# Kernel tuning notes

Hardware: AMD Instinct MI355X
Metric: run time of the kernel (lower is better)

## Reference

```python
import jax, jax.numpy as jnp
import numpy as np

B, C, Q, T, D = 16, 6, 256, 256, 256
NUM_IDS = 300
IMG_H = IMG_W = 512


def setup_inputs() -> dict:
    key = jax.random.key(0)
    ks = jax.random.split(key, 8)
    det_tokens = jax.random.normal(ks[0], (B, C, Q, D), jnp.float32)
    det_scores = jax.random.uniform(ks[1], (B, C, Q), jnp.float32)
    det_boxes = jax.random.uniform(ks[2], (B, C, Q, 4), jnp.float32)
    assoc = jax.nn.softmax(jax.random.normal(ks[3], (B, C, Q, T), jnp.float32), axis=-1)
    cam_mask = jax.random.uniform(ks[4], (B, C)) < 0.9
    target_mask = jax.random.uniform(ks[5], (B, C, Q)) < 0.5
    ids = jax.random.randint(ks[6], (B, C, Q), 0, NUM_IDS)
    boxes = jax.random.uniform(ks[7], (B, C, Q, 4), jnp.float32) * IMG_W
    return {"det_tokens": det_tokens, "det_scores": det_scores, "det_boxes": det_boxes,
            "assoc": assoc, "boxes": boxes, "cam_mask": cam_mask,
            "target_mask": target_mask, "ids": ids, "img_h": IMG_H, "img_w": IMG_W}


def _masked_mean(x, m):
    w = m.astype(x.dtype)
    return (x * w).sum() / jnp.maximum(w.sum(), 1.0)


def _pack(ids, target_mask, cam_mask, q_count):
    # Vectorized version of _query_ids_from_targets: stable-compact valid targets
    # to the front of the query axis (preserves original order, as boolean indexing does).
    order = jnp.argsort(jnp.where(target_mask, 0, 1), axis=-1, stable=True)  # valid first
    sids = jnp.take_along_axis(ids, order, axis=-1)[..., :q_count]
    count = target_mask.sum(axis=-1)  # [B,C]
    qvalid = (jnp.arange(q_count)[None, None, :] < count[..., None]) & cam_mask[..., None]
    qids = jnp.where(qvalid, sids, -1)
    return qids, qvalid, order


def reference(det_tokens, det_scores, det_boxes, assoc, boxes, cam_mask, target_mask, ids, img_h, img_w):
    Bq, Cc, Qn, Tn = assoc.shape
    qids, qvalid, order = _pack(ids, target_mask, cam_mask, Qn)

    # det_norm
    det_norm = jnp.mean(det_tokens ** 2)

    # detector supervision (masked BCE on scores + masked L1 on boxes)
    norm = jnp.array([img_w, img_h, img_w, img_h], det_boxes.dtype)
    box_gt = boxes / norm  # [B,C,maxT,4]
    sboxes = jnp.take_along_axis(box_gt, order[..., None], axis=2)[:, :, :Qn]
    obj_target = qvalid.astype(det_scores.dtype)
    box_target = jnp.where(qvalid[..., None], jnp.clip(sboxes, 0.0, 1.0), 0.0)
    p = jnp.clip(det_scores, 1e-6, 1.0 - 1e-6)
    bce = -(obj_target * jnp.log(p) + (1.0 - obj_target) * jnp.log1p(-p))
    cam3 = jnp.broadcast_to(cam_mask[:, :, None], bce.shape)
    score_loss = _masked_mean(bce, cam3)
    box_loss = _masked_mean(jnp.abs(det_boxes - box_target),
                            jnp.broadcast_to(qvalid[..., None], det_boxes.shape))
    det_supervision = score_loss + box_loss

    # assoc entropy (masked by camera validity)
    logp_full = jnp.log(jnp.maximum(assoc, 1e-8))
    entropy = -(logp_full * assoc).sum(-1)  # [B,C,Q]
    assoc_entropy_loss = _masked_mean(entropy, jnp.broadcast_to(cam_mask[:, :, None], entropy.shape))

    # assoc supervised NLL over track slots
    slots = jnp.remainder(jnp.maximum(qids, 0), Tn)  # [B,C,Q]
    nll = -jnp.take_along_axis(logp_full, slots[..., None], axis=-1)[..., 0]
    assoc_pair_loss = _masked_mean(nll, qvalid)

    # cross-view consistency: broadcasted id-equality replaces quadruple python loop
    eq = qids[:, :, None, :, None] == qids[:, None, :, None, :]       # [B,c1,c2,q1,q2]
    pv = qvalid[:, :, None, :, None] & qvalid[:, None, :, None, :]
    tri = jnp.triu(jnp.ones((Cc, Cc), bool), 1)[None, :, :, None, None]  # c1 < c2
    M = (eq & pv & tri).astype(assoc.dtype)
    cnt = M.sum(-1)  # [B,c1,c2,q1]
    peer = jnp.einsum('bcdqp,bdpt->bcdqt', M, assoc) / jnp.maximum(cnt, 1.0)[..., None]
    ref = assoc[:, :, None, :, :]
    term = jnp.mean((ref - peer) ** 2, axis=-1)  # per-pair MSE over track slots
    assoc_consistency = _masked_mean(term, cnt > 0)

    total = det_norm + det_supervision + assoc_entropy_loss + assoc_pair_loss + assoc_consistency
    return total, det_norm, det_supervision, assoc_entropy_loss, assoc_pair_loss, assoc_consistency
```

## Files before the change

### kernel.cpp

```cpp
#include <hip/hip_runtime.h>
#include <math.h>

#define BB 16
#define CC 6
#define QQ 256
#define TT 256
#define DD 256
#define NPAIR 15
#define NBC (BB * CC)
#define CONS_BLOCKS (BB * NPAIR * 4)
#define PACK_BLOCKS NBC
#define BIG_BLOCKS (NBC * 8)
#define MAIN_BLOCKS (CONS_BLOCKS + PACK_BLOCKS + BIG_BLOCKS)


__device__ __forceinline__ float block_sum256(float v, float* s_red) {
    #pragma unroll
    for (int off = 32; off > 0; off >>= 1) v += __shfl_xor(v, off, 64);
    __syncthreads();
    if ((threadIdx.x & 63) == 0) s_red[threadIdx.x >> 6] = v;
    __syncthreads();
    return s_red[0] + s_red[1] + s_red[2] + s_red[3];
}

__device__ __forceinline__ float2 block_sum256x2(float a, float b, float2* s_red2) {
    #pragma unroll
    for (int off = 32; off > 0; off >>= 1) {
        a += __shfl_xor(a, off, 64);
        b += __shfl_xor(b, off, 64);
    }
    __syncthreads();
    if ((threadIdx.x & 63) == 0) s_red2[threadIdx.x >> 6] = make_float2(a, b);
    __syncthreads();
    float2 r;
    r.x = s_red2[0].x + s_red2[1].x + s_red2[2].x + s_red2[3].x;
    r.y = s_red2[0].y + s_red2[1].y + s_red2[2].y + s_red2[3].y;
    return r;
}

__device__ __forceinline__ int read_bool(const void* p, int idx, int fmt) {
    if (fmt == 2) return ((const float*)p)[idx] != 0.0f;
    if (fmt == 1) return ((const unsigned char*)p)[idx] != 0;
    return ((const int*)p)[idx] != 0;
}

__device__ __forceinline__ int detect_fmt(const void* tm_raw, int* s_cf, int* s_cm) {
    const int t = threadIdx.x;
    if (t == 0) { *s_cf = 0; *s_cm = 0; }
    __syncthreads();
    uint4 w = ((const uint4*)tm_raw)[t];
    unsigned int u4[4] = {w.x, w.y, w.z, w.w};
    int cf = 0, cm = 0;
    #pragma unroll
    for (int k = 0; k < 4; k++) {
        cf += ((u4[k] >> 24) == 0x3Fu);
        cm += ((u4[k] & 0xFFFFFF00u) != 0u);
    }
    if (cf) atomicAdd(s_cf, cf);
    if (cm) atomicAdd(s_cm, cm);
    __syncthreads();
    return (*s_cf > 16) ? 2 : ((*s_cm > 0) ? 1 : 0);
}

__device__ __forceinline__ int block_pack(const void* tm_raw,
                                          const int* __restrict__ ids,
                                          int bc, int fmt, int cam,
                                          int* s_sids, int* s_wsum,
                                          int* s_out) {
    const int t = threadIdx.x, lane = t & 63, wv = t >> 6;
    const int tm = read_bool(tm_raw, bc * QQ + t, fmt);
    int v = tm;
    #pragma unroll
    for (int off = 1; off < 64; off <<= 1) {
        int u = __shfl_up(v, off, 64);
        if (lane >= off) v += u;
    }
    if (lane == 63) s_wsum[wv] = v;
    __syncthreads();
    const int count = s_wsum[0] + s_wsum[1] + s_wsum[2] + s_wsum[3];
    int woff = 0;
    #pragma unroll
    for (int k = 0; k < 3; k++) woff += (k < wv) ? s_wsum[k] : 0;
    const int excl = woff + v - tm;
    const int rank = tm ? excl : (count + (t - excl));
    s_sids[rank] = ids[bc * QQ + t];
    __syncthreads();
    s_out[t] = (t < count && cam) ? s_sids[t] : -1;
    __syncthreads();
    return count;
}

__global__ __launch_bounds__(256)
void k_main(const float4* __restrict__ tok,
            const float* __restrict__ assoc,
            const float* __restrict__ det_scores,
            const float* __restrict__ det_boxes,
            const float* __restrict__ boxes,
            const void* __restrict__ cam_raw,
            const void* __restrict__ tm_raw,
            const int* __restrict__ ids,
            const int* __restrict__ img_h_p,
            const int* __restrict__ img_w_p,
            float* __restrict__ packPart,
            float* __restrict__ bigPart,
            float* __restrict__ consPart) {
    const int blk = blockIdx.x;
    const int t = threadIdx.x, lane = t & 63, wv = t >> 6;
    __shared__ int s_cf, s_cm;
    __shared__ float2 s_red2[4];

    if (blk >= CONS_BLOCKS + PACK_BLOCKS) {
        const int bb = blk - (CONS_BLOCKS + PACK_BLOCKS);
        const int bc = bb >> 3;
        const long base = (long)bc * 16384 + (long)(bb & 7) * 2048 + t;
        const float4* asc = (const float4*)assoc;
        const int fmt = detect_fmt(tm_raw, &s_cf, &s_cm);
        const int cam = read_bool(cam_raw, bc, fmt);

        float ss = 0.0f, ent = 0.0f;
        #pragma unroll
        for (int h = 0; h < 2; h++) {
            const long o = base + h * 1024;
            float4 t0 = tok[o], t1 = tok[o + 256], t2 = tok[o + 512], t3 = tok[o + 768];
            float4 a0 = asc[o], a1 = asc[o + 256], a2 = asc[o + 512], a3 = asc[o + 768];
            ss += t0.x * t0.x + t0.y * t0.y + t0.z * t0.z + t0.w * t0.w
                + t1.x * t1.x + t1.y * t1.y + t1.z * t1.z + t1.w * t1.w
                + t2.x * t2.x + t2.y * t2.y + t2.z * t2.z + t2.w * t2.w
                + t3.x * t3.x + t3.y * t3.y + t3.z * t3.z + t3.w * t3.w;
            if (cam) {
                ent -= a0.x * __logf(fmaxf(a0.x, 1e-8f)) + a0.y * __logf(fmaxf(a0.y, 1e-8f))
                     + a0.z * __logf(fmaxf(a0.z, 1e-8f)) + a0.w * __logf(fmaxf(a0.w, 1e-8f));
                ent -= a1.x * __logf(fmaxf(a1.x, 1e-8f)) + a1.y * __logf(fmaxf(a1.y, 1e-8f))
                     + a1.z * __logf(fmaxf(a1.z, 1e-8f)) + a1.w * __logf(fmaxf(a1.w, 1e-8f));
                ent -= a2.x * __logf(fmaxf(a2.x, 1e-8f)) + a2.y * __logf(fmaxf(a2.y, 1e-8f))
                     + a2.z * __logf(fmaxf(a2.z, 1e-8f)) + a2.w * __logf(fmaxf(a2.w, 1e-8f));
                ent -= a3.x * __logf(fmaxf(a3.x, 1e-8f)) + a3.y * __logf(fmaxf(a3.y, 1e-8f))
                     + a3.z * __logf(fmaxf(a3.z, 1e-8f)) + a3.w * __logf(fmaxf(a3.w, 1e-8f));
            }
        }
        float2 r = block_sum256x2(ss, ent, s_red2);
        if (t == 0) { bigPart[bb * 2] = r.x; bigPart[bb * 2 + 1] = r.y; }

    } else if (blk >= CONS_BLOCKS) {
        const int bc = blk - CONS_BLOCKS;
        __shared__ int s_sids[QQ], s_qid[QQ], s_wsum[4];
        const int fmt = detect_fmt(tm_raw, &s_cf, &s_cm);
        const int cam = read_bool(cam_raw, bc, fmt);
        const int count = block_pack(tm_raw, ids, bc, fmt, cam, s_sids, s_wsum, s_qid);
        const int tm = read_bool(tm_raw, bc * QQ + t, fmt);
        int v = tm;
        #pragma unroll
        for (int off = 1; off < 64; off <<= 1) {
            int u = __shfl_up(v, off, 64);
            if (lane >= off) v += u;
        }
        int woff = 0;
        #pragma unroll
        for (int k = 0; k < 3; k++) woff += (k < wv) ? s_wsum[k] : 0;
        const int excl = woff + v - tm;
        const int rank = tm ? excl : (count + (t - excl));

        const int j = t;
        const int qv = (j < count) && cam;
        const int qid = s_qid[j];

        float score_sum = 0.0f, box_sum = 0.0f, pair_sum = 0.0f;
        if (cam) {
            float p = det_scores[(size_t)bc * QQ + j];
            p = fminf(fmaxf(p, 1e-6f), 1.0f - 1e-6f);
            score_sum = (j < count) ? -__logf(p) : -__logf(1.0f - p);
        }
        if (qv) {
            int slot = qid & (TT - 1);
            float a = assoc[((size_t)bc * QQ + j) * TT + slot];
            pair_sum = -__logf(fmaxf(a, 1e-8f));
        }
        if (tm && cam) {
            const int jj = rank;
            const float iw = (float)img_w_p[0], ih = (float)img_h_p[0];
            const float* bx = boxes + ((size_t)bc * QQ + t) * 4;
            const float* db = det_boxes + ((size_t)bc * QQ + jj) * 4;
            float b0 = fminf(fmaxf(bx[0] / iw, 0.0f), 1.0f);
            float b1 = fminf(fmaxf(bx[1] / ih, 0.0f), 1.0f);
            float b2 = fminf(fmaxf(bx[2] / iw, 0.0f), 1.0f);
            float b3 = fminf(fmaxf(bx[3] / ih, 0.0f), 1.0f);
            box_sum = fabsf(db[0] - b0) + fabsf(db[1] - b1) +
                      fabsf(db[2] - b2) + fabsf(db[3] - b3);
        }
        float2 r1 = block_sum256x2(score_sum, box_sum, s_red2);
        float2 r2 = block_sum256x2(pair_sum, 0.0f, s_red2);
        if (t == 0) {
            float* row = packPart + bc * 8;
            row[0] = r1.x; row[1] = r1.y; row[2] = r2.x;
            row[3] = cam ? (float)count : 0.0f;
            row[4] = (float)cam;
        }

    } else {
        const int cb = blk;
        const int qg = cb & 3;
        const int bp = cb >> 2;
        const int b = bp / NPAIR;
        int pi = bp % NPAIR;
        int c = 0, d = 1;
        {
            int k = pi;
            for (c = 0; c < CC - 1; c++) {
                int span = CC - 1 - c;
                if (k < span) { d = c + 1 + k; break; }
                k -= span;
            }
        }
        __shared__ int s_sids[QQ], s_qc[QQ], s_qd[QQ], s_wsum[4];
        const int fmt = detect_fmt(tm_raw, &s_cf, &s_cm);
        const int cam_c = read_bool(cam_raw, b * CC + c, fmt);
        const int cam_d = read_bool(cam_raw, b * CC + d, fmt);
        block_pack(tm_raw, ids, b * CC + c, fmt, cam_c, s_sids, s_wsum, s_qc);
        block_pack(tm_raw, ids, b * CC + d, fmt, cam_d, s_sids, s_wsum, s_qd);

        const int qd0 = s_qd[lane];
        const int qd1 = s_qd[64 + lane];
        const int qd2 = s_qd[128 + lane];
        const int qd3 = s_qd[192 + lane];
        int idarr[16];
        #pragma unroll
        for (int qi = 0; qi < 16; qi++) idarr[qi] = s_qc[qg * 64 + wv * 16 + qi];

        const float4* assoc_c = (const float4*)(assoc + (size_t)(b * CC + c) * QQ * TT);
        const float4* assoc_d = (const float4*)(assoc + (size_t)(b * CC + d) * QQ * TT);

        float tot = 0.0f, nval = 0.0f;
        #pragma unroll 4
        for (int qi = 0; qi < 16; qi++) {
            const int id = idarr[qi];
            if (id < 0) continue;
            unsigned long long m0 = __ballot(qd0 == id);
            unsigned long long m1 = __ballot(qd1 == id);
            unsigned long long m2 = __ballot(qd2 == id);
            unsigned long long m3 = __ballot(qd3 == id);
            int cnt = __popcll(m0) + __popcll(m1) + __popcll(m2) + __popcll(m3);
            if (cnt == 0) continue;
            const int q = qg * 64 + wv * 16 + qi;
            float4 r = assoc_c[(size_t)q * (TT / 4) + lane];
            float ax = 0.0f, ay = 0.0f, az = 0.0f, aw = 0.0f;
            unsigned long long mm[4] = {m0, m1, m2, m3};
            #pragma unroll
            for (int kk = 0; kk < 4; kk++) {
                unsigned long long m = mm[kk];
                while (m) {
                    int p = kk * 64 + __builtin_ctzll(m);
                    m &= m - 1;
                    float4 vv = assoc_d[(size_t)p * (TT / 4) + lane];
                    ax += vv.x; ay += vv.y; az += vv.z; aw += vv.w;
                }
            }
            float inv = 1.0f / (float)cnt;
            float dx = r.x - ax * inv, dy = r.y - ay * inv;
            float dz = r.z - az * inv, dw = r.w - aw * inv;
            tot += dx * dx + dy * dy + dz * dz + dw * dw;
            nval += 1.0f;
        }
        float2 r2 = block_sum256x2(tot, nval, s_red2);
        if (t == 0) {
            consPart[cb * 2] = r2.x * (1.0f / TT);
            consPart[cb * 2 + 1] = r2.y;
        }
    }
}

__global__ __launch_bounds__(256)
void k_fin(const float* __restrict__ packPart, const float2* __restrict__ bigPart,
           const float2* __restrict__ consPart, float* __restrict__ out) {
    const int t = threadIdx.x;
    __shared__ float s_red[4];
    float sc = 0, bx = 0, pr = 0, qv = 0, cm = 0;
    if (t < NBC) {
        const float* row = packPart + t * 8;
        sc = row[0]; bx = row[1]; pr = row[2]; qv = row[3]; cm = row[4];
    }
    float ss = 0, ent = 0;
    #pragma unroll
    for (int k = 0; k < BIG_BLOCKS / 256; k++) {
        float2 v = bigPart[k * 256 + t];
        ss += v.x; ent += v.y;
    }
    float cons = 0, nval = 0;
    for (int i = t; i < CONS_BLOCKS; i += 256) {
        float2 v = consPart[i];
        cons += v.x; nval += v.y;
    }
    sc = block_sum256(sc, s_red);
    bx = block_sum256(bx, s_red);
    pr = block_sum256(pr, s_red);
    qv = block_sum256(qv, s_red);
    cm = block_sum256(cm, s_red);
    ss = block_sum256(ss, s_red);
    ent = block_sum256(ent, s_red);
    cons = block_sum256(cons, s_red);
    nval = block_sum256(nval, s_red);
    if (t == 0) {
        float det_norm = ss / (float)((long)BB * CC * QQ * DD);
        float denom_cam = fmaxf(cm * (float)QQ, 1.0f);
        float score_loss = sc / denom_cam;
        float box_loss = bx / fmaxf(4.0f * qv, 1.0f);
        float det_sup = score_loss + box_loss;
        float ent_loss = ent / denom_cam;
        float pair_loss = pr / fmaxf(qv, 1.0f);
        float cons_loss = cons / fmaxf(nval, 1.0f);
        out[0] = det_norm + det_sup + ent_loss + pair_loss + cons_loss;
        out[1] = det_norm;
        out[2] = det_sup;
        out[3] = ent_loss;
        out[4] = pair_loss;
        out[5] = cons_loss;
    }
}

extern "C" void kernel_launch(void* const* d_in, const int* in_sizes, int n_in,
                              void* d_out, int out_size, void* d_ws, size_t ws_size,
                              hipStream_t stream) {
    const float* det_tokens = (const float*)d_in[0];
    const float* det_scores = (const float*)d_in[1];
    const float* det_boxes  = (const float*)d_in[2];
    const float* assoc      = (const float*)d_in[3];
    const float* boxes      = (const float*)d_in[4];
    const void*  cam_raw    = d_in[5];
    const void*  tm_raw     = d_in[6];
    const int*   ids        = (const int*)d_in[7];
    const int*   img_h      = (const int*)d_in[8];
    const int*   img_w      = (const int*)d_in[9];

    char* ws = (char*)d_ws;
    float* packPart = (float*)(ws + 0);
    float* bigPart  = (float*)(ws + 4096);
    float* consPart = (float*)(ws + 16384);

    k_main<<<MAIN_BLOCKS, 256, 0, stream>>>((const float4*)det_tokens, assoc,
                                            det_scores, det_boxes, boxes,
                                            cam_raw, tm_raw, ids, img_h, img_w,
                                            packPart, bigPart, consPart);
    k_fin<<<1, 256, 0, stream>>>(packPart, (const float2*)bigPart,
                                 (const float2*)consPart, (float*)d_out);
}
```

Baseline: 112.4 us.

## Reorder block roles, wave-level format detection, fused pack scans and reductions

Block roles are reordered so the bandwidth-heavy streaming blocks come first, followed by consistency blocks and then pack blocks. The shared-memory atomic format detection is replaced with per-wave ballots, which removes two barriers from every block. The two prefix-sum packs in consistency blocks are fused into one pass, det_tokens is read with nontemporal loads, assoc loads are skipped for inactive cameras, and the final and pack reductions are merged into single multi-value reductions. These cut barrier and latency overhead, at the cost of more code and register pressure.

```diff
diff --git a/kernel.cpp b/kernel.cpp
--- a/kernel.cpp
+++ b/kernel.cpp
@@ -8,11 +8,13 @@
 #define DD 256
 #define NPAIR 15
 #define NBC (BB * CC)
-#define CONS_BLOCKS (BB * NPAIR * 4)
-#define PACK_BLOCKS NBC
-#define BIG_BLOCKS (NBC * 8)
-#define MAIN_BLOCKS (CONS_BLOCKS + PACK_BLOCKS + BIG_BLOCKS)
-
+#define BIGB (NBC * 8)
+#define CONSB (BB * NPAIR * 4)
+#define PACKB NBC
+#define MAIN_BLOCKS (BIGB + CONSB + PACKB)
+
+
+typedef float f4 __attribute__((ext_vector_type(4)));
 
 __device__ __forceinline__ float block_sum256(float v, float* s_red) {
     #pragma unroll
@@ -38,60 +40,88 @@
     return r;
 }
 
+__device__ __forceinline__ float4 block_sum256x4(float a, float b, float c,
+                                                 float d, float4* s_red4) {
+    #pragma unroll
+    for (int off = 32; off > 0; off >>= 1) {
+        a += __shfl_xor(a, off, 64);
+        b += __shfl_xor(b, off, 64);
+        c += __shfl_xor(c, off, 64);
+        d += __shfl_xor(d, off, 64);
+    }
+    __syncthreads();
+    if ((threadIdx.x & 63) == 0) s_red4[threadIdx.x >> 6] = make_float4(a, b, c, d);
+    __syncthreads();
+    float4 r;
+    r.x = s_red4[0].x + s_red4[1].x + s_red4[2].x + s_red4[3].x;
+    r.y = s_red4[0].y + s_red4[1].y + s_red4[2].y + s_red4[3].y;
+    r.z = s_red4[0].z + s_red4[1].z + s_red4[2].z + s_red4[3].z;
+    r.w = s_red4[0].w + s_red4[1].w + s_red4[2].w + s_red4[3].w;
+    return r;
+}
+
 __device__ __forceinline__ int read_bool(const void* p, int idx, int fmt) {
     if (fmt == 2) return ((const float*)p)[idx] != 0.0f;
     if (fmt == 1) return ((const unsigned char*)p)[idx] != 0;
     return ((const int*)p)[idx] != 0;
 }
 
-__device__ __forceinline__ int detect_fmt(const void* tm_raw, int* s_cf, int* s_cm) {
-    const int t = threadIdx.x;
-    if (t == 0) { *s_cf = 0; *s_cm = 0; }
-    __syncthreads();
-    uint4 w = ((const uint4*)tm_raw)[t];
-    unsigned int u4[4] = {w.x, w.y, w.z, w.w};
-    int cf = 0, cm = 0;
-    #pragma unroll
-    for (int k = 0; k < 4; k++) {
-        cf += ((u4[k] >> 24) == 0x3Fu);
-        cm += ((u4[k] & 0xFFFFFF00u) != 0u);
-    }
-    if (cf) atomicAdd(s_cf, cf);
-    if (cm) atomicAdd(s_cm, cm);
-    __syncthreads();
-    return (*s_cf > 16) ? 2 : ((*s_cm > 0) ? 1 : 0);
-}
-
-__device__ __forceinline__ int block_pack(const void* tm_raw,
-                                          const int* __restrict__ ids,
-                                          int bc, int fmt, int cam,
-                                          int* s_sids, int* s_wsum,
-                                          int* s_out) {
+__device__ __forceinline__ int detect_fmt_wave(const void* tm_raw) {
+    const int lane = threadIdx.x & 63;
+    uint4 w = ((const uint4*)tm_raw)[lane];
+    unsigned long long f0 = __ballot((w.x >> 24) == 0x3Fu);
+    unsigned long long f1 = __ballot((w.y >> 24) == 0x3Fu);
+    unsigned long long f2 = __ballot((w.z >> 24) == 0x3Fu);
+    unsigned long long f3 = __ballot((w.w >> 24) == 0x3Fu);
+    int cf = __popcll(f0) + __popcll(f1) + __popcll(f2) + __popcll(f3);
+    unsigned long long m0 = __ballot((w.x & 0xFFFFFF00u) != 0u);
+    unsigned long long m1 = __ballot((w.y & 0xFFFFFF00u) != 0u);
+    unsigned long long m2 = __ballot((w.z & 0xFFFFFF00u) != 0u);
+    unsigned long long m3 = __ballot((w.w & 0xFFFFFF00u) != 0u);
+    int cm = __popcll(m0) | __popcll(m1) | __popcll(m2) | __popcll(m3);
+    return (cf > 16) ? 2 : ((cm > 0) ? 1 : 0);
+}
+
+__device__ __forceinline__ void block_pack2(const void* tm_raw,
+                                            const int* __restrict__ ids,
+                                            int bc_c, int bc_d, int fmt,
+                                            int cam_c, int cam_d,
+                                            int* s_tmp, int* s_wsum,
+                                            int* s_qc, int* s_qd,
+                                            int& count_c, int& count_d) {
     const int t = threadIdx.x, lane = t & 63, wv = t >> 6;
-    const int tm = read_bool(tm_raw, bc * QQ + t, fmt);
-    int v = tm;
+    const int tmc = read_bool(tm_raw, bc_c * QQ + t, fmt);
+    const int tmd = read_bool(tm_raw, bc_d * QQ + t, fmt);
+    int vc = tmc, vd = tmd;
     #pragma unroll
     for (int off = 1; off < 64; off <<= 1) {
-        int u = __shfl_up(v, off, 64);
-        if (lane >= off) v += u;
-    }
-    if (lane == 63) s_wsum[wv] = v;
-    __syncthreads();
-    const int count = s_wsum[0] + s_wsum[1] + s_wsum[2] + s_wsum[3];
-    int woff = 0;
-    #pragma unroll
-    for (int k = 0; k < 3; k++) woff += (k < wv) ? s_wsum[k] : 0;
-    const int excl = woff + v - tm;
-    const int rank = tm ? excl : (count + (t - excl));
-    s_sids[rank] = ids[bc * QQ + t];
-    __syncthreads();
-    s_out[t] = (t < count && cam) ? s_sids[t] : -1;
-    __syncthreads();
-    return count;
+        int uc = __shfl_up(vc, off, 64);
+        int ud = __shfl_up(vd, off, 64);
+        if (lane >= off) { vc += uc; vd += ud; }
+    }
+    if (lane == 63) { s_wsum[wv] = vc; s_wsum[4 + wv] = vd; }
+    __syncthreads();
+    count_c = s_wsum[0] + s_wsum[1] + s_wsum[2] + s_wsum[3];
+    count_d = s_wsum[4] + s_wsum[5] + s_wsum[6] + s_wsum[7];
+    int woc = 0, wod = 0;
+    #pragma unroll
+    for (int k = 0; k < 3; k++) {
+        if (k < wv) { woc += s_wsum[k]; wod += s_wsum[4 + k]; }
+    }
+    const int exc = woc + vc - tmc;
+    const int exd = wod + vd - tmd;
+    const int rc = tmc ? exc : (count_c + (t - exc));
+    const int rd = tmd ? exd : (count_d + (t - exd));
+    s_tmp[rc] = ids[bc_c * QQ + t];
+    s_tmp[QQ + rd] = ids[bc_d * QQ + t];
+    __syncthreads();
+    s_qc[t] = (t < count_c && cam_c) ? s_tmp[t] : -1;
+    s_qd[t] = (t < count_d && cam_d) ? s_tmp[QQ + t] : -1;
+    __syncthreads();
 }
 
 __global__ __launch_bounds__(256)
-void k_main(const float4* __restrict__ tok,
+void k_main(const f4* __restrict__ tok,
             const float* __restrict__ assoc,
             const float* __restrict__ det_scores,
             const float* __restrict__ det_boxes,
@@ -106,28 +136,30 @@
             float* __restrict__ consPart) {
     const int blk = blockIdx.x;
     const int t = threadIdx.x, lane = t & 63, wv = t >> 6;
-    __shared__ int s_cf, s_cm;
     __shared__ float2 s_red2[4];
 
-    if (blk >= CONS_BLOCKS + PACK_BLOCKS) {
-        const int bb = blk - (CONS_BLOCKS + PACK_BLOCKS);
+    if (blk < BIGB) {
+        const int bb = blk;
         const int bc = bb >> 3;
         const long base = (long)bc * 16384 + (long)(bb & 7) * 2048 + t;
-        const float4* asc = (const float4*)assoc;
-        const int fmt = detect_fmt(tm_raw, &s_cf, &s_cm);
+        const f4* asc = (const f4*)assoc;
+        const int fmt = detect_fmt_wave(tm_raw);
         const int cam = read_bool(cam_raw, bc, fmt);
 
         float ss = 0.0f, ent = 0.0f;
         #pragma unroll
         for (int h = 0; h < 2; h++) {
             const long o = base + h * 1024;
-            float4 t0 = tok[o], t1 = tok[o + 256], t2 = tok[o + 512], t3 = tok[o + 768];
-            float4 a0 = asc[o], a1 = asc[o + 256], a2 = asc[o + 512], a3 = asc[o + 768];
+            f4 t0 = __builtin_nontemporal_load(&tok[o]);
+            f4 t1 = __builtin_nontemporal_load(&tok[o + 256]);
+            f4 t2 = __builtin_nontemporal_load(&tok[o + 512]);
+            f4 t3 = __builtin_nontemporal_load(&tok[o + 768]);
             ss += t0.x * t0.x + t0.y * t0.y + t0.z * t0.z + t0.w * t0.w
                 + t1.x * t1.x + t1.y * t1.y + t1.z * t1.z + t1.w * t1.w
                 + t2.x * t2.x + t2.y * t2.y + t2.z * t2.z + t2.w * t2.w
                 + t3.x * t3.x + t3.y * t3.y + t3.z * t3.z + t3.w * t3.w;
             if (cam) {
+                f4 a0 = asc[o], a1 = asc[o + 256], a2 = asc[o + 512], a3 = asc[o + 768];
                 ent -= a0.x * __logf(fmaxf(a0.x, 1e-8f)) + a0.y * __logf(fmaxf(a0.y, 1e-8f))
                      + a0.z * __logf(fmaxf(a0.z, 1e-8f)) + a0.w * __logf(fmaxf(a0.w, 1e-8f));
                 ent -= a1.x * __logf(fmaxf(a1.x, 1e-8f)) + a1.y * __logf(fmaxf(a1.y, 1e-8f))
@@ -141,63 +173,8 @@
         float2 r = block_sum256x2(ss, ent, s_red2);
         if (t == 0) { bigPart[bb * 2] = r.x; bigPart[bb * 2 + 1] = r.y; }
 
-    } else if (blk >= CONS_BLOCKS) {
-        const int bc = blk - CONS_BLOCKS;
-        __shared__ int s_sids[QQ], s_qid[QQ], s_wsum[4];
-        const int fmt = detect_fmt(tm_raw, &s_cf, &s_cm);
-        const int cam = read_bool(cam_raw, bc, fmt);
-        const int count = block_pack(tm_raw, ids, bc, fmt, cam, s_sids, s_wsum, s_qid);
-        const int tm = read_bool(tm_raw, bc * QQ + t, fmt);
-        int v = tm;
-        #pragma unroll
-        for (int off = 1; off < 64; off <<= 1) {
-            int u = __shfl_up(v, off, 64);
-            if (lane >= off) v += u;
-        }
-        int woff = 0;
-        #pragma unroll
-        for (int k = 0; k < 3; k++) woff += (k < wv) ? s_wsum[k] : 0;
-        const int excl = woff + v - tm;
-        const int rank = tm ? excl : (count + (t - excl));
-
-        const int j = t;
-        const int qv = (j < count) && cam;
-        const int qid = s_qid[j];
-
-        float score_sum = 0.0f, box_sum = 0.0f, pair_sum = 0.0f;
-        if (cam) {
-            float p = det_scores[(size_t)bc * QQ + j];
-            p = fminf(fmaxf(p, 1e-6f), 1.0f - 1e-6f);
-            score_sum = (j < count) ? -__logf(p) : -__logf(1.0f - p);
-        }
-        if (qv) {
-            int slot = qid & (TT - 1);
-            float a = assoc[((size_t)bc * QQ + j) * TT + slot];
-            pair_sum = -__logf(fmaxf(a, 1e-8f));
-        }
-        if (tm && cam) {
-            const int jj = rank;
-            const float iw = (float)img_w_p[0], ih = (float)img_h_p[0];
-            const float* bx = boxes + ((size_t)bc * QQ + t) * 4;
-            const float* db = det_boxes + ((size_t)bc * QQ + jj) * 4;
-            float b0 = fminf(fmaxf(bx[0] / iw, 0.0f), 1.0f);
-            float b1 = fminf(fmaxf(bx[1] / ih, 0.0f), 1.0f);
-            float b2 = fminf(fmaxf(bx[2] / iw, 0.0f), 1.0f);
-            float b3 = fminf(fmaxf(bx[3] / ih, 0.0f), 1.0f);
-            box_sum = fabsf(db[0] - b0) + fabsf(db[1] - b1) +
-                      fabsf(db[2] - b2) + fabsf(db[3] - b3);
-        }
-        float2 r1 = block_sum256x2(score_sum, box_sum, s_red2);
-        float2 r2 = block_sum256x2(pair_sum, 0.0f, s_red2);
-        if (t == 0) {
-            float* row = packPart + bc * 8;
-            row[0] = r1.x; row[1] = r1.y; row[2] = r2.x;
-            row[3] = cam ? (float)count : 0.0f;
-            row[4] = (float)cam;
-        }
-
-    } else {
-        const int cb = blk;
+    } else if (blk < BIGB + CONSB) {
+        const int cb = blk - BIGB;
         const int qg = cb & 3;
         const int bp = cb >> 2;
         const int b = bp / NPAIR;
@@ -211,12 +188,13 @@
                 k -= span;
             }
         }
-        __shared__ int s_sids[QQ], s_qc[QQ], s_qd[QQ], s_wsum[4];
-        const int fmt = detect_fmt(tm_raw, &s_cf, &s_cm);
+        __shared__ int s_tmp[2 * QQ], s_qc[QQ], s_qd[QQ], s_wsum[8];
+        const int fmt = detect_fmt_wave(tm_raw);
         const int cam_c = read_bool(cam_raw, b * CC + c, fmt);
         const int cam_d = read_bool(cam_raw, b * CC + d, fmt);
-        block_pack(tm_raw, ids, b * CC + c, fmt, cam_c, s_sids, s_wsum, s_qc);
-        block_pack(tm_raw, ids, b * CC + d, fmt, cam_d, s_sids, s_wsum, s_qd);
+        int count_c, count_d;
+        block_pack2(tm_raw, ids, b * CC + c, b * CC + d, fmt, cam_c, cam_d,
+                    s_tmp, s_wsum, s_qc, s_qd, count_c, count_d);
 
         const int qd0 = s_qd[lane];
         const int qd1 = s_qd[64 + lane];
@@ -226,8 +204,8 @@
         #pragma unroll
         for (int qi = 0; qi < 16; qi++) idarr[qi] = s_qc[qg * 64 + wv * 16 + qi];
 
-        const float4* assoc_c = (const float4*)(assoc + (size_t)(b * CC + c) * QQ * TT);
-        const float4* assoc_d = (const float4*)(assoc + (size_t)(b * CC + d) * QQ * TT);
+        const f4* assoc_c = (const f4*)(assoc + (size_t)(b * CC + c) * QQ * TT);
+        const f4* assoc_d = (const f4*)(assoc + (size_t)(b * CC + d) * QQ * TT);
 
         float tot = 0.0f, nval = 0.0f;
         #pragma unroll 4
@@ -241,7 +219,7 @@
             int cnt = __popcll(m0) + __popcll(m1) + __popcll(m2) + __popcll(m3);
             if (cnt == 0) continue;
             const int q = qg * 64 + wv * 16 + qi;
-            float4 r = assoc_c[(size_t)q * (TT / 4) + lane];
+            f4 r = assoc_c[(size_t)q * (TT / 4) + lane];
             float ax = 0.0f, ay = 0.0f, az = 0.0f, aw = 0.0f;
             unsigned long long mm[4] = {m0, m1, m2, m3};
             #pragma unroll
@@ -250,7 +228,7 @@
                 while (m) {
                     int p = kk * 64 + __builtin_ctzll(m);
                     m &= m - 1;
-                    float4 vv = assoc_d[(size_t)p * (TT / 4) + lane];
+                    f4 vv = assoc_d[(size_t)p * (TT / 4) + lane];
                     ax += vv.x; ay += vv.y; az += vv.z; aw += vv.w;
                 }
             }
@@ -265,40 +243,111 @@
             consPart[cb * 2] = r2.x * (1.0f / TT);
             consPart[cb * 2 + 1] = r2.y;
         }
+
+    } else {
+        const int bc = blk - (BIGB + CONSB);
+        __shared__ int s_sids[QQ], s_wsum[4];
+        __shared__ float4 s_red4[4];
+        const int fmt = detect_fmt_wave(tm_raw);
+        const int cam = read_bool(cam_raw, bc, fmt);
+
+        const int tm = read_bool(tm_raw, bc * QQ + t, fmt);
+        int v = tm;
+        #pragma unroll
+        for (int off = 1; off < 64; off <<= 1) {
+            int u = __shfl_up(v, off, 64);
+            if (lane >= off) v += u;
+        }
+        if (lane == 63) s_wsum[wv] = v;
+        __syncthreads();
+        const int count = s_wsum[0] + s_wsum[1] + s_wsum[2] + s_wsum[3];
+        int woff = 0;
+        #pragma unroll
+        for (int k = 0; k < 3; k++) woff += (k < wv) ? s_wsum[k] : 0;
+        const int excl = woff + v - tm;
+        const int rank = tm ? excl : (count + (t - excl));
+        s_sids[rank] = ids[bc * QQ + t];
+        __syncthreads();
+
+        const int j = t;
+        const int qv = (j < count) && cam;
+        const int qid = qv ? s_sids[j] : -1;
+
+        float score_sum = 0.0f, box_sum = 0.0f, pair_sum = 0.0f;
+        if (cam) {
+            float p = det_scores[(size_t)bc * QQ + j];
+            p = fminf(fmaxf(p, 1e-6f), 1.0f - 1e-6f);
+            score_sum = (j < count) ? -__logf(p) : -__logf(1.0f - p);
+        }
+        if (qv) {
+            int slot = qid & (TT - 1);
+            float a = assoc[((size_t)bc * QQ + j) * TT + slot];
+            pair_sum = -__logf(fmaxf(a, 1e-8f));
+        }
+        if (tm && cam) {
+            const int jj = rank;
+            const float iw = (float)img_w_p[0], ih = (float)img_h_p[0];
+            const float* bx = boxes + ((size_t)bc * QQ + t) * 4;
+            const float* db = det_boxes + ((size_t)bc * QQ + jj) * 4;
+            float b0 = fminf(fmaxf(bx[0] / iw, 0.0f), 1.0f);
+            float b1 = fminf(fmaxf(bx[1] / ih, 0.0f), 1.0f);
+            float b2 = fminf(fmaxf(bx[2] / iw, 0.0f), 1.0f);
+            float b3 = fminf(fmaxf(bx[3] / ih, 0.0f), 1.0f);
+            box_sum = fabsf(db[0] - b0) + fabsf(db[1] - b1) +
+                      fabsf(db[2] - b2) + fabsf(db[3] - b3);
+        }
+        float4 r = block_sum256x4(score_sum, box_sum, pair_sum, 0.0f, s_red4);
+        if (t == 0) {
+            float* row = packPart + bc * 8;
+            row[0] = r.x; row[1] = r.y; row[2] = r.z;
+            row[3] = cam ? (float)count : 0.0f;
+            row[4] = (float)cam;
+        }
     }
 }
 
 __global__ __launch_bounds__(256)
 void k_fin(const float* __restrict__ packPart, const float2* __restrict__ bigPart,
            const float2* __restrict__ consPart, float* __restrict__ out) {
-    const int t = threadIdx.x;
-    __shared__ float s_red[4];
-    float sc = 0, bx = 0, pr = 0, qv = 0, cm = 0;
+    const int t = threadIdx.x, lane = t & 63, wv = t >> 6;
+    __shared__ float s_r[4][9];
+    float vals[9];
+    #pragma unroll
+    for (int k = 0; k < 9; k++) vals[k] = 0.0f;
     if (t < NBC) {
         const float* row = packPart + t * 8;
-        sc = row[0]; bx = row[1]; pr = row[2]; qv = row[3]; cm = row[4];
-    }
-    float ss = 0, ent = 0;
-    #pragma unroll
-    for (int k = 0; k < BIG_BLOCKS / 256; k++) {
+        vals[0] = row[0]; vals[1] = row[1]; vals[2] = row[2];
+        vals[3] = row[3]; vals[4] = row[4];
+    }
+    #pragma unroll
+    for (int k = 0; k < BIGB / 256; k++) {
         float2 v = bigPart[k * 256 + t];
-        ss += v.x; ent += v.y;
-    }
-    float cons = 0, nval = 0;
-    for (int i = t; i < CONS_BLOCKS; i += 256) {
+        vals[5] += v.x; vals[6] += v.y;
+    }
+    for (int i = t; i < CONSB; i += 256) {
         float2 v = consPart[i];
-        cons += v.x; nval += v.y;
-    }
-    sc = block_sum256(sc, s_red);
-    bx = block_sum256(bx, s_red);
-    pr = block_sum256(pr, s_red);
-    qv = block_sum256(qv, s_red);
-    cm = block_sum256(cm, s_red);
-    ss = block_sum256(ss, s_red);
-    ent = block_sum256(ent, s_red);
-    cons = block_sum256(cons, s_red);
-    nval = block_sum256(nval, s_red);
+        vals[7] += v.x; vals[8] += v.y;
+    }
+    #pragma unroll
+    for (int off = 32; off > 0; off >>= 1) {
+        #pragma unroll
+        for (int k = 0; k < 9; k++) vals[k] += __shfl_xor(vals[k], off, 64);
+    }
+    if (lane == 0) {
+        #pragma unroll
+        for (int k = 0; k < 9; k++) s_r[wv][k] = vals[k];
+    }
+    __syncthreads();
     if (t == 0) {
+        float sc   = s_r[0][0] + s_r[1][0] + s_r[2][0] + s_r[3][0];
+        float bx   = s_r[0][1] + s_r[1][1] + s_r[2][1] + s_r[3][1];
+        float pr   = s_r[0][2] + s_r[1][2] + s_r[2][2] + s_r[3][2];
+        float qv   = s_r[0][3] + s_r[1][3] + s_r[2][3] + s_r[3][3];
+        float cm   = s_r[0][4] + s_r[1][4] + s_r[2][4] + s_r[3][4];
+        float ss   = s_r[0][5] + s_r[1][5] + s_r[2][5] + s_r[3][5];
+        float ent  = s_r[0][6] + s_r[1][6] + s_r[2][6] + s_r[3][6];
+        float cons = s_r[0][7] + s_r[1][7] + s_r[2][7] + s_r[3][7];
+        float nval = s_r[0][8] + s_r[1][8] + s_r[2][8] + s_r[3][8];
         float det_norm = ss / (float)((long)BB * CC * QQ * DD);
         float denom_cam = fmaxf(cm * (float)QQ, 1.0f);
         float score_loss = sc / denom_cam;
@@ -335,7 +384,7 @@
     float* bigPart  = (float*)(ws + 4096);
     float* consPart = (float*)(ws + 16384);
 
-    k_main<<<MAIN_BLOCKS, 256, 0, stream>>>((const float4*)det_tokens, assoc,
+    k_main<<<MAIN_BLOCKS, 256, 0, stream>>>((const f4*)det_tokens, assoc,
                                             det_scores, det_boxes, boxes,
                                             cam_raw, tm_raw, ids, img_h, img_w,
                                             packPart, bigPart, consPart);
```

Result: no change. 112.8 us (+0.3%).
